# Kernel optimization log

Measured on AMD Instinct MI355X. Metric: run time of the kernel, lower is better.

The kernel has to match this reference:

```python
import jax, jax.numpy as jnp
import numpy as np

C = 256
G = 32  # GroupNorm groups
EPS = 1e-6


def setup_inputs() -> dict:
    key = jax.random.key(0)
    ks = jax.random.split(key, 10)
    b, c, d, h, w = 2, C, 16, 16, 16
    s = 1.0 / np.sqrt(c)
    return {
        "x": jax.random.normal(ks[0], (b, c, d, h, w), jnp.float32),
        "gn_gamma": jnp.ones((c,), jnp.float32),
        "gn_beta": jnp.zeros((c,), jnp.float32),
        "wq": jax.random.normal(ks[1], (c, c), jnp.float32) * s,
        "bq": jax.random.normal(ks[2], (c,), jnp.float32) * 0.01,
        "wk": jax.random.normal(ks[3], (c, c), jnp.float32) * s,
        "bk": jax.random.normal(ks[4], (c,), jnp.float32) * 0.01,
        "wv": jax.random.normal(ks[5], (c, c), jnp.float32) * s,
        "bv": jax.random.normal(ks[6], (c,), jnp.float32) * 0.01,
        "wp": jax.random.normal(ks[7], (c, c), jnp.float32) * s,
        "bp": jax.random.normal(ks[8], (c,), jnp.float32) * 0.01,
    }


def _group_norm(x, gamma, beta):
    b, c, d, h, w = x.shape
    xg = x.reshape(b, G, c // G, d, h, w)
    mu = jnp.mean(xg, axis=(2, 3, 4, 5), keepdims=True)
    var = jnp.var(xg, axis=(2, 3, 4, 5), keepdims=True)
    xn = ((xg - mu) * jax.lax.rsqrt(var + EPS)).reshape(b, c, d, h, w)
    return xn * gamma[None, :, None, None, None] + beta[None, :, None, None, None]


def reference(x, gn_gamma, gn_beta, wq, bq, wk, bk, wv, bv, wp, bp):
    b, c, d, h, w = x.shape
    n = d * h * w
    hn = _group_norm(x, gn_gamma, gn_beta).reshape(b, c, n)  # (b, c, n)
    # 1x1 conv3d == channel-mixing matmul
    q = jnp.einsum("oc,bcn->bon", wq, hn) + bq[None, :, None]
    k = jnp.einsum("oc,bcn->bon", wk, hn) + bk[None, :, None]
    v = jnp.einsum("oc,bcn->bon", wv, hn) + bv[None, :, None]
    scale = c ** (-0.5)
    attn = jax.nn.softmax(jnp.einsum("bcn,bcm->bnm", q, k) * scale, axis=2)  # (b, n, m)
    # torch: h_ = bmm(v, attn^T) -> h_[b,c,n] = sum_m v[b,c,m] * attn[b,n,m]
    hv = jnp.einsum("bcm,bnm->bcn", v, attn)
    out = jnp.einsum("oc,bcn->bon", wp, hv) + bp[None, :, None]
    w_returned = jnp.transpose(attn, (0, 2, 1))  # matches torch's returned permuted w_
    return (x + out.reshape(b, c, d, h, w), w_returned)
```

## Files before the change

### kernel.cpp

```cpp
#include <hip/hip_runtime.h>


typedef __bf16 bf16_t;
typedef __bf16 bf16x8 __attribute__((ext_vector_type(8)));
typedef float floatx4 __attribute__((ext_vector_type(4)));

__device__ __forceinline__ unsigned short f2bf(float f) {
  union { float f; unsigned int u; } v; v.f = f;
  return (unsigned short)((v.u + 0x7FFFu + ((v.u >> 16) & 1u)) >> 16);
}
__device__ __forceinline__ float bf2f(unsigned short u) {
  union { unsigned int u; float f; } v; v.u = ((unsigned int)u) << 16;
  return v.f;
}

__global__ void prep_kernel(const float* __restrict__ wq, const float* __restrict__ wk,
                            const float* __restrict__ wv, const float* __restrict__ wp,
                            const float* __restrict__ bq, const float* __restrict__ bk,
                            const float* __restrict__ bv, const float* __restrict__ bp,
                            const float* __restrict__ x, unsigned short* __restrict__ Astack,
                            unsigned short* __restrict__ wpbf, unsigned short* __restrict__ wvT,
                            float* __restrict__ bqkv2, float* __restrict__ bias2,
                            float* __restrict__ mean, float* __restrict__ rstd) {
  __shared__ float T[64 * 67];
  __shared__ float red[256];
  const int blk = blockIdx.x;
  const int tid = threadIdx.x;
  if (blk < 768) {
    int w = blk >> 8;
    const float* src = (w == 0) ? wq : (w == 1) ? wk : wp;
    unsigned short* dst = (w == 0) ? Astack : (w == 1) ? (Astack + 65536) : wpbf;
    int i = (blk & 255) * 256 + tid;
    dst[i] = f2bf(src[i]);
  } else if (blk < 784) {
    int t = blk - 768, tr = t >> 2, tc = t & 3;
#pragma unroll
    for (int rr = 0; rr < 16; ++rr) {
      int r = rr * 4 + (tid >> 6), c = tid & 63;
      T[r * 67 + c] = wv[(size_t)(tr * 64 + r) * 256 + tc * 64 + c];
    }
    __syncthreads();
#pragma unroll
    for (int rr = 0; rr < 16; ++rr) {
      int cc = rr * 4 + (tid >> 6), r = tid & 63;
      wvT[(size_t)(tc * 64 + cc) * 256 + tr * 64 + r] = f2bf(T[r * 67 + cc]);
    }
  } else if (blk < 848) {
    int bg = blk - 784;
    const float* p = x + (size_t)bg * 32768;
    float s = 0.f, ss = 0.f;
    for (int i = tid * 4; i < 32768; i += 1024) {
      float4 v = *(const float4*)&p[i];
      s += v.x + v.y + v.z + v.w;
      ss += v.x * v.x + v.y * v.y + v.z * v.z + v.w * v.w;
    }
    for (int off = 32; off > 0; off >>= 1) {
      s += __shfl_down(s, off);
      ss += __shfl_down(ss, off);
    }
    int wid = tid >> 6;
    if ((tid & 63) == 0) { red[wid] = s; red[64 + wid] = ss; }
    __syncthreads();
    if (tid == 0) {
      float S = red[0] + red[1] + red[2] + red[3];
      float SS = red[64] + red[65] + red[66] + red[67];
      float mu = S * (1.f / 32768.f);
      float var = SS * (1.f / 32768.f) - mu * mu;
      mean[bg] = mu;
      rstd[bg] = rsqrtf(var + 1e-6f);
    }
  } else if (blk == 848) {
    bqkv2[tid] = bq[tid];
    bqkv2[256 + tid] = bk[tid];
    bqkv2[512 + tid] = 0.f;
  } else {
    int bb = blk - 849;
    int o = bb * 64 + (tid >> 2), part = tid & 3;
    float s = 0.f;
#pragma unroll
    for (int j = 0; j < 16; ++j) {
      float4 w4 = *(const float4*)&wp[(size_t)o * 256 + part * 64 + j * 4];
      float4 b4 = *(const float4*)&bv[part * 64 + j * 4];
      s += w4.x * b4.x + w4.y * b4.y + w4.z * b4.z + w4.w * b4.w;
    }
    red[tid] = s;
    __syncthreads();
    if (part == 0) bias2[o] = bp[o] + red[tid] + red[tid + 1] + red[tid + 2] + red[tid + 3];
  }
}

__global__ void gn_apply_t_kernel(const float* __restrict__ x, const float* __restrict__ gamma,
                                  const float* __restrict__ beta, const float* __restrict__ mean,
                                  const float* __restrict__ rstd, unsigned short* __restrict__ hnT) {
  int n0 = blockIdx.x * 64, c0 = blockIdx.y * 64, b = blockIdx.z;
  int tid = threadIdx.x;
  __shared__ __align__(16) unsigned short T[64 * 72];
#pragma unroll
  for (int r = 0; r < 4; ++r) {
    int cl = (tid >> 4) + r * 16;
    int nl = (tid & 15) * 4;
    int c = c0 + cl;
    int bg = b * 32 + (c >> 3);
    float mu = mean[bg], rs = rstd[bg], ga = gamma[c], be = beta[c];
    float4 v = *(const float4*)&x[(size_t)b * 1048576 + (size_t)c * 4096 + n0 + nl];
    ushort4 u;
    u.x = f2bf((v.x - mu) * rs * ga + be);
    u.y = f2bf((v.y - mu) * rs * ga + be);
    u.z = f2bf((v.z - mu) * rs * ga + be);
    u.w = f2bf((v.w - mu) * rs * ga + be);
    *(ushort4*)&T[cl * 72 + nl] = u;
  }
  __syncthreads();
#pragma unroll
  for (int w = 0; w < 2; ++w) {
    int nl = (tid >> 3) + w * 32;
    int cch = (tid & 7) * 8;
    unsigned short u8[8];
#pragma unroll
    for (int i = 0; i < 8; ++i) u8[i] = T[(cch + i) * 72 + nl];
    size_t o = (size_t)b * 1048576 + (size_t)(n0 + nl) * 256 + c0 + cch;
    *(ushort4*)&hnT[o] = make_ushort4(u8[0], u8[1], u8[2], u8[3]);
    *(ushort4*)&hnT[o + 4] = make_ushort4(u8[4], u8[5], u8[6], u8[7]);
  }
}

template <int BM, int BN>
__launch_bounds__(256)
__global__ void gemm_tn(const bf16_t* __restrict__ A, const bf16_t* __restrict__ B, int ldb,
                        unsigned short* __restrict__ C, int N, int K) {
  constexpr int BK = 32, LD = BK + 8;
  constexpr int WM = BM / 2, WN = BN / 2, MI = WM / 16, NI = WN / 16;
  __shared__ __align__(16) bf16_t As[BM * LD];
  __shared__ __align__(16) bf16_t Bs[BN * LD];
  const int tid = threadIdx.x;
  const int lane = tid & 63, wid = tid >> 6;
  const int quad = lane >> 4, l16 = lane & 15;
  const int m0 = blockIdx.y * BM, n0 = blockIdx.x * BN;
  const int wm0 = (wid >> 1) * WM, wn0 = (wid & 1) * WN;

  floatx4 acc[MI][NI];
#pragma unroll
  for (int i = 0; i < MI; ++i)
#pragma unroll
    for (int j = 0; j < NI; ++j) acc[i][j] = (floatx4){0.f, 0.f, 0.f, 0.f};

  const int arow = tid >> 2, akj = (tid & 3) << 3;
  for (int kt = 0; kt < K; kt += BK) {
#pragma unroll
    for (int p = 0; p < BM / 64; ++p) {
      int r = p * 64 + arow;
      *(uint4*)&As[r * LD + akj] = *(const uint4*)&A[(size_t)(m0 + r) * K + kt + akj];
    }
#pragma unroll
    for (int p = 0; p < BN / 64; ++p) {
      int r = p * 64 + arow;
      *(uint4*)&Bs[r * LD + akj] = *(const uint4*)&B[(size_t)(n0 + r) * ldb + kt + akj];
    }
    __syncthreads();
    bf16x8 af[MI], bfr[NI];
#pragma unroll
    for (int i = 0; i < MI; ++i) af[i] = *(const bf16x8*)&As[(wm0 + i * 16 + l16) * LD + quad * 8];
#pragma unroll
    for (int j = 0; j < NI; ++j) bfr[j] = *(const bf16x8*)&Bs[(wn0 + j * 16 + l16) * LD + quad * 8];
#pragma unroll
    for (int i = 0; i < MI; ++i)
#pragma unroll
      for (int j = 0; j < NI; ++j)
        acc[i][j] = __builtin_amdgcn_mfma_f32_16x16x32_bf16(af[i], bfr[j], acc[i][j], 0, 0, 0);
    __syncthreads();
  }

#pragma unroll
  for (int i = 0; i < MI; ++i) {
    int gmb = m0 + wm0 + i * 16 + quad * 4;
#pragma unroll
    for (int j = 0; j < NI; ++j) {
      int gn = n0 + wn0 + j * 16 + l16;
#pragma unroll
      for (int r = 0; r < 4; ++r) C[(size_t)(gmb + r) * N + gn] = f2bf(acc[i][j][r]);
    }
  }
}

__launch_bounds__(256)
__global__ void gemm_qkvw(const bf16_t* __restrict__ Astack, const bf16_t* __restrict__ hnT,
                          const float* __restrict__ bqkv2, unsigned short* __restrict__ qkT,
                          unsigned short* __restrict__ W2) {
  constexpr int BM = 64, BN = 128, BK = 32, LD = BK + 8, MI = 2, NI = 4;
  __shared__ __align__(16) bf16_t As[BM * LD];
  __shared__ __align__(16) bf16_t Bs[BN * LD];
  const int tid = threadIdx.x;
  const int lane = tid & 63, wid = tid >> 6;
  const int quad = lane >> 4, l16 = lane & 15;
  const int b = blockIdx.z;
  const bf16_t* B = hnT + (size_t)b * 1048576;
  const int m0 = blockIdx.y * BM, n0 = blockIdx.x * BN;
  const int wm0 = (wid >> 1) * 32, wn0 = (wid & 1) * 64;

  floatx4 acc[MI][NI];
#pragma unroll
  for (int i = 0; i < MI; ++i)
#pragma unroll
    for (int j = 0; j < NI; ++j) acc[i][j] = (floatx4){0.f, 0.f, 0.f, 0.f};

  const int arow = tid >> 2, akj = (tid & 3) << 3;
  for (int kt = 0; kt < 256; kt += BK) {
    {
      int r = arow;
      *(uint4*)&As[r * LD + akj] = *(const uint4*)&Astack[(size_t)(m0 + r) * 256 + kt + akj];
    }
#pragma unroll
    for (int p = 0; p < 2; ++p) {
      int r = p * 64 + arow;
      *(uint4*)&Bs[r * LD + akj] = *(const uint4*)&B[(size_t)(n0 + r) * 256 + kt + akj];
    }
    __syncthreads();
    bf16x8 af[MI], bfr[NI];
#pragma unroll
    for (int i = 0; i < MI; ++i) af[i] = *(const bf16x8*)&As[(wm0 + i * 16 + l16) * LD + quad * 8];
#pragma unroll
    for (int j = 0; j < NI; ++j) bfr[j] = *(const bf16x8*)&Bs[(wn0 + j * 16 + l16) * LD + quad * 8];
#pragma unroll
    for (int i = 0; i < MI; ++i)
#pragma unroll
      for (int j = 0; j < NI; ++j)
        acc[i][j] = __builtin_amdgcn_mfma_f32_16x16x32_bf16(af[i], bfr[j], acc[i][j], 0, 0, 0);
    __syncthreads();
  }

#pragma unroll
  for (int i = 0; i < MI; ++i) {
    int gmb = m0 + wm0 + i * 16 + quad * 4;
#pragma unroll
    for (int j = 0; j < NI; ++j) {
      int gn = n0 + wn0 + j * 16 + l16;
      float v[4];
#pragma unroll
      for (int r = 0; r < 4; ++r) v[r] = acc[i][j][r] + bqkv2[gmb + r];
      if (m0 < 512) {
        ushort4 u = make_ushort4(f2bf(v[0]), f2bf(v[1]), f2bf(v[2]), f2bf(v[3]));
        *(ushort4*)&qkT[(size_t)b * 2097152 + (size_t)gn * 512 + gmb] = u;
      } else {
#pragma unroll
        for (int r = 0; r < 4; ++r)
          W2[(size_t)b * 1048576 + (size_t)(gmb - 512 + r) * 4096 + gn] = f2bf(v[r]);
      }
    }
  }
}

__launch_bounds__(256)
__global__ void gemm_qk_exp(const bf16_t* __restrict__ qkT, unsigned short* __restrict__ EbfT,
                            float* __restrict__ psum) {
  constexpr int BM = 128, BN = 128, BK = 32, LD = BK + 8, MI = 4, NI = 4;
  constexpr int LDC = BM + 8;
  __shared__ __align__(16) char SMEM[BM * LDC * 2];
  bf16_t* As = (bf16_t*)SMEM;
  bf16_t* Bs = (bf16_t*)SMEM + BM * LD;
  unsigned short* Ct = (unsigned short*)SMEM;
  const int tid = threadIdx.x;
  const int lane = tid & 63, wid = tid >> 6;
  const int quad = lane >> 4, l16 = lane & 15;
  const int b = blockIdx.z;
  const bf16_t* A = qkT + (size_t)b * 2097152 + 256;
  const bf16_t* B = qkT + (size_t)b * 2097152;
  const int m0 = blockIdx.y * BM, n0 = blockIdx.x * BN;
  const int wm0 = (wid >> 1) * 64, wn0 = (wid & 1) * 64;

  floatx4 acc[MI][NI];
#pragma unroll
  for (int i = 0; i < MI; ++i)
#pragma unroll
    for (int j = 0; j < NI; ++j) acc[i][j] = (floatx4){0.f, 0.f, 0.f, 0.f};

  const int arow = tid >> 2, akj = (tid & 3) << 3;
  for (int kt = 0; kt < 256; kt += BK) {
#pragma unroll
    for (int p = 0; p < 2; ++p) {
      int r = p * 64 + arow;
      *(uint4*)&As[r * LD + akj] = *(const uint4*)&A[(size_t)(m0 + r) * 512 + kt + akj];
      *(uint4*)&Bs[r * LD + akj] = *(const uint4*)&B[(size_t)(n0 + r) * 512 + kt + akj];
    }
    __syncthreads();
    bf16x8 af[MI], bfr[NI];
#pragma unroll
    for (int i = 0; i < MI; ++i) af[i] = *(const bf16x8*)&As[(wm0 + i * 16 + l16) * LD + quad * 8];
#pragma unroll
    for (int j = 0; j < NI; ++j) bfr[j] = *(const bf16x8*)&Bs[(wn0 + j * 16 + l16) * LD + quad * 8];
#pragma unroll
    for (int i = 0; i < MI; ++i)
#pragma unroll
      for (int j = 0; j < NI; ++j)
        acc[i][j] = __builtin_amdgcn_mfma_f32_16x16x32_bf16(af[i], bfr[j], acc[i][j], 0, 0, 0);
    __syncthreads();
  }

  float csum[NI] = {0.f, 0.f, 0.f, 0.f};
#pragma unroll
  for (int i = 0; i < MI; ++i) {
    int ml = wm0 + i * 16 + quad * 4;
#pragma unroll
    for (int j = 0; j < NI; ++j) {
      int nl = wn0 + j * 16 + l16;
      float e[4];
#pragma unroll
      for (int r = 0; r < 4; ++r) e[r] = __expf(acc[i][j][r] * 0.0625f);
      csum[j] += (e[0] + e[1]) + (e[2] + e[3]);
      *(ushort4*)&Ct[nl * LDC + ml] = make_ushort4(f2bf(e[0]), f2bf(e[1]), f2bf(e[2]), f2bf(e[3]));
    }
  }
#pragma unroll
  for (int j = 0; j < NI; ++j) {
    csum[j] += __shfl_xor(csum[j], 16);
    csum[j] += __shfl_xor(csum[j], 32);
  }
  if (quad == 0) {
    int my = blockIdx.y * 2 + (wid >> 1);
#pragma unroll
    for (int j = 0; j < NI; ++j)
      psum[((size_t)b * 64 + my) * 4096 + n0 + wn0 + j * 16 + l16] = csum[j];
  }
  __syncthreads();
#pragma unroll
  for (int pass = 0; pass < 8; ++pass) {
    int row = pass * 16 + (tid >> 4);
    int mc = (tid & 15) * 8;
    uint4 v = *(uint4*)&Ct[row * LDC + mc];
    *(uint4*)&EbfT[(size_t)b * 16777216 + (size_t)(n0 + row) * 4096 + m0 + mc] = v;
  }
}

__launch_bounds__(256)
__global__ void gemm_pv_fused(const bf16_t* __restrict__ W2, const bf16_t* __restrict__ EbfT,
                              const float* __restrict__ psum, const float* __restrict__ bias2,
                              const float* __restrict__ x, float* __restrict__ out0,
                              float* __restrict__ attn) {
  constexpr int BK = 64, LDA = 72, LDB = 72;
  __shared__ __align__(16) bf16_t As[128 * LDA];
  __shared__ __align__(16) bf16_t Bs[32 * LDB];
  __shared__ float rs[32];
  __shared__ float sred[256];
  const int tid = threadIdx.x;
  const int lane = tid & 63, wid = tid >> 6;
  const int quad = lane >> 4, l16 = lane & 15;
  const int b = blockIdx.z, mb = blockIdx.y;
  const int n0 = blockIdx.x * 32;
  const size_t eb = (size_t)b * 16777216;

  {
    int nl = tid & 31, rp = tid >> 5;
    float s = 0.f;
#pragma unroll
    for (int i = 0; i < 8; ++i) s += psum[((size_t)b * 64 + rp * 8 + i) * 4096 + n0 + nl];
    sred[tid] = s;
  }
  __syncthreads();
  if (tid < 32) {
    float s = 0.f;
#pragma unroll
    for (int i = 0; i < 8; ++i) s += sred[i * 32 + tid];
    rs[tid] = 1.f / s;
  }
  __syncthreads();

  const int wm0 = (wid >> 1) * 64, wn0 = (wid & 1) * 16;
  floatx4 acc[4];
#pragma unroll
  for (int i = 0; i < 4; ++i) acc[i] = (floatx4){0.f, 0.f, 0.f, 0.f};

  for (int kt = 0; kt < 4096; kt += BK) {
#pragma unroll
    for (int p = 0; p < 4; ++p) {
      int r = p * 32 + (tid >> 3);
      int kk = (tid & 7) * 8;
      *(uint4*)&As[r * LDA + kk] =
          *(const uint4*)&W2[(size_t)b * 1048576 + (size_t)(mb * 128 + r) * 4096 + kt + kk];
    }
    {
      int r = tid >> 3;
      int kk = (tid & 7) * 8;
      *(uint4*)&Bs[r * LDB + kk] = *(const uint4*)&EbfT[eb + (size_t)(n0 + r) * 4096 + kt + kk];
    }
    __syncthreads();
    {
      int ml = mb * 32 + (tid >> 3);
      int n4 = (tid & 7) * 4;
      const unsigned short* Bu = (const unsigned short*)Bs;
      float4 o;
      o.x = bf2f(Bu[(n4 + 0) * LDB + ml]) * rs[n4 + 0];
      o.y = bf2f(Bu[(n4 + 1) * LDB + ml]) * rs[n4 + 1];
      o.z = bf2f(Bu[(n4 + 2) * LDB + ml]) * rs[n4 + 2];
      o.w = bf2f(Bu[(n4 + 3) * LDB + ml]) * rs[n4 + 3];
      *(float4*)&attn[eb + (size_t)(kt + ml) * 4096 + n0 + n4] = o;
    }
    bf16x8 af[2][4], bfr[2];
#pragma unroll
    for (int ks = 0; ks < 2; ++ks) {
      bfr[ks] = *(const bf16x8*)&Bs[(wn0 + l16) * LDB + ks * 32 + quad * 8];
#pragma unroll
      for (int i = 0; i < 4; ++i)
        af[ks][i] = *(const bf16x8*)&As[(wm0 + i * 16 + l16) * LDA + ks * 32 + quad * 8];
    }
#pragma unroll
    for (int ks = 0; ks < 2; ++ks)
#pragma unroll
      for (int i = 0; i < 4; ++i)
        acc[i] = __builtin_amdgcn_mfma_f32_16x16x32_bf16(af[ks][i], bfr[ks], acc[i], 0, 0, 0);
    __syncthreads();
  }

  const float* xb = x + (size_t)b * 1048576;
  float* ob = out0 + (size_t)b * 1048576;
  int gn = n0 + wn0 + l16;
  float cs = rs[wn0 + l16];
#pragma unroll
  for (int i = 0; i < 4; ++i) {
    int o = mb * 128 + wm0 + i * 16 + quad * 4;
#pragma unroll
    for (int r = 0; r < 4; ++r)
      ob[(size_t)(o + r) * 4096 + gn] =
          acc[i][r] * cs + bias2[o + r] + xb[(size_t)(o + r) * 4096 + gn];
  }
}

extern "C" void kernel_launch(void* const* d_in, const int* in_sizes, int n_in,
                              void* d_out, int out_size, void* d_ws, size_t ws_size,
                              hipStream_t stream) {
  const float* x = (const float*)d_in[0];
  const float* gamma = (const float*)d_in[1];
  const float* beta = (const float*)d_in[2];
  const float* wq = (const float*)d_in[3];
  const float* bq = (const float*)d_in[4];
  const float* wk = (const float*)d_in[5];
  const float* bk = (const float*)d_in[6];
  const float* wv = (const float*)d_in[7];
  const float* bv = (const float*)d_in[8];
  const float* wp = (const float*)d_in[9];
  const float* bp = (const float*)d_in[10];

  float* out0 = (float*)d_out;
  float* attn = (float*)d_out + 2097152;

  char* ws = (char*)d_ws;
  unsigned short* Astack = (unsigned short*)(ws + 0);
  unsigned short* wpbf = (unsigned short*)(ws + 393216);
  unsigned short* wvT = (unsigned short*)(ws + 524288);
  float* bqkv2 = (float*)(ws + 655360);
  float* bias2 = (float*)(ws + 658432);
  float* gmean = (float*)(ws + 659456);
  float* grstd = (float*)(ws + 659712);
  float* psum = (float*)(ws + 1048576);
  unsigned short* hnT = (unsigned short*)(ws + 4194304);
  unsigned short* qkT = (unsigned short*)(ws + 8388608);
  unsigned short* W2 = (unsigned short*)(ws + 16777216);
  unsigned short* EbfT = (unsigned short*)(ws + 20971520);

  prep_kernel<<<853, 256, 0, stream>>>(wq, wk, wv, wp, bq, bk, bv, bp, x, Astack, wpbf, wvT,
                                       bqkv2, bias2, gmean, grstd);

  gemm_tn<64, 128><<<dim3(2, 4, 1), 256, 0, stream>>>((const bf16_t*)wpbf, (const bf16_t*)wvT, 256,
                                                      Astack + 131072, 256, 256);

  gn_apply_t_kernel<<<dim3(64, 4, 2), 256, 0, stream>>>(x, gamma, beta, gmean, grstd, hnT);

  gemm_qkvw<<<dim3(32, 12, 2), 256, 0, stream>>>((const bf16_t*)Astack, (const bf16_t*)hnT, bqkv2,
                                                 qkT, W2);

  gemm_qk_exp<<<dim3(32, 32, 2), 256, 0, stream>>>((const bf16_t*)qkT, EbfT, psum);

  gemm_pv_fused<<<dim3(128, 2, 2), 256, 0, stream>>>((const bf16_t*)W2, (const bf16_t*)EbfT, psum,
                                                     bias2, x, out0, attn);
}
```

Before: 278.0 us.

## Use direct global-to-LDS loads with XOR-swizzled tiles and larger K blocks

The three GEMM kernels now stage tiles with global_load_lds (16-byte direct-to-LDS copies) instead of loading through registers, and use XOR-swizzled unpadded LDS layouts to avoid bank conflicts. The K tile grows to 64 in the QKV and QK kernels and to 128 in the PV kernel, which halves the number of barriers per tile. The attention-weight write in the PV kernel is reindexed to read the swizzled layout and to store 8 floats per thread. This removes register staging and VGPR pressure, at the cost of more LDS use and swizzle address arithmetic.

```diff
diff --git a/kernel.cpp b/kernel.cpp
--- a/kernel.cpp
+++ b/kernel.cpp
@@ -4,6 +4,13 @@
 typedef __bf16 bf16_t;
 typedef __bf16 bf16x8 __attribute__((ext_vector_type(8)));
 typedef float floatx4 __attribute__((ext_vector_type(4)));
+
+typedef __attribute__((address_space(1))) const unsigned int gas_u32;
+typedef __attribute__((address_space(3))) unsigned int las_u32;
+
+__device__ __forceinline__ void gl_lds16(const void* g, void* l) {
+  __builtin_amdgcn_global_load_lds((gas_u32*)g, (las_u32*)l, 16, 0, 0);
+}
 
 __device__ __forceinline__ unsigned short f2bf(float f) {
   union { float f; unsigned int u; } v; v.f = f;
@@ -101,13 +108,13 @@
     int nl = (tid & 15) * 4;
     int c = c0 + cl;
     int bg = b * 32 + (c >> 3);
-    float mu = mean[bg], rs = rstd[bg], ga = gamma[c], be = beta[c];
+    float mu = mean[bg], rsd = rstd[bg], ga = gamma[c], be = beta[c];
     float4 v = *(const float4*)&x[(size_t)b * 1048576 + (size_t)c * 4096 + n0 + nl];
     ushort4 u;
-    u.x = f2bf((v.x - mu) * rs * ga + be);
-    u.y = f2bf((v.y - mu) * rs * ga + be);
-    u.z = f2bf((v.z - mu) * rs * ga + be);
-    u.w = f2bf((v.w - mu) * rs * ga + be);
+    u.x = f2bf((v.x - mu) * rsd * ga + be);
+    u.y = f2bf((v.y - mu) * rsd * ga + be);
+    u.z = f2bf((v.z - mu) * rsd * ga + be);
+    u.w = f2bf((v.w - mu) * rsd * ga + be);
     *(ushort4*)&T[cl * 72 + nl] = u;
   }
   __syncthreads();
@@ -186,9 +193,9 @@
 __global__ void gemm_qkvw(const bf16_t* __restrict__ Astack, const bf16_t* __restrict__ hnT,
                           const float* __restrict__ bqkv2, unsigned short* __restrict__ qkT,
                           unsigned short* __restrict__ W2) {
-  constexpr int BM = 64, BN = 128, BK = 32, LD = BK + 8, MI = 2, NI = 4;
-  __shared__ __align__(16) bf16_t As[BM * LD];
-  __shared__ __align__(16) bf16_t Bs[BN * LD];
+  constexpr int BM = 64, BN = 128, BK = 64, MI = 2, NI = 4;
+  __shared__ __align__(16) bf16_t As[BM * BK];
+  __shared__ __align__(16) bf16_t Bs[BN * BK];
   const int tid = threadIdx.x;
   const int lane = tid & 63, wid = tid >> 6;
   const int quad = lane >> 4, l16 = lane & 15;
@@ -196,6 +203,8 @@
   const bf16_t* B = hnT + (size_t)b * 1048576;
   const int m0 = blockIdx.y * BM, n0 = blockIdx.x * BN;
   const int wm0 = (wid >> 1) * 32, wn0 = (wid & 1) * 64;
+  const int srow = lane >> 3;
+  const int scol = ((lane & 7) ^ srow) << 3;
 
   floatx4 acc[MI][NI];
 #pragma unroll
@@ -203,28 +212,37 @@
 #pragma unroll
     for (int j = 0; j < NI; ++j) acc[i][j] = (floatx4){0.f, 0.f, 0.f, 0.f};
 
-  const int arow = tid >> 2, akj = (tid & 3) << 3;
   for (int kt = 0; kt < 256; kt += BK) {
-    {
-      int r = arow;
-      *(uint4*)&As[r * LD + akj] = *(const uint4*)&Astack[(size_t)(m0 + r) * 256 + kt + akj];
-    }
 #pragma unroll
     for (int p = 0; p < 2; ++p) {
-      int r = p * 64 + arow;
-      *(uint4*)&Bs[r * LD + akj] = *(const uint4*)&B[(size_t)(n0 + r) * 256 + kt + akj];
-    }
-    __syncthreads();
-    bf16x8 af[MI], bfr[NI];
-#pragma unroll
-    for (int i = 0; i < MI; ++i) af[i] = *(const bf16x8*)&As[(wm0 + i * 16 + l16) * LD + quad * 8];
-#pragma unroll
-    for (int j = 0; j < NI; ++j) bfr[j] = *(const bf16x8*)&Bs[(wn0 + j * 16 + l16) * LD + quad * 8];
-#pragma unroll
-    for (int i = 0; i < MI; ++i)
-#pragma unroll
-      for (int j = 0; j < NI; ++j)
-        acc[i][j] = __builtin_amdgcn_mfma_f32_16x16x32_bf16(af[i], bfr[j], acc[i][j], 0, 0, 0);
+      int rb = wid * 16 + p * 8;
+      gl_lds16(&Astack[(size_t)(m0 + rb + srow) * 256 + kt + scol], &As[rb * BK]);
+    }
+#pragma unroll
+    for (int p = 0; p < 4; ++p) {
+      int rb = wid * 32 + p * 8;
+      gl_lds16(&B[(size_t)(n0 + rb + srow) * 256 + kt + scol], &Bs[rb * BK]);
+    }
+    __syncthreads();
+#pragma unroll
+    for (int ks = 0; ks < 2; ++ks) {
+      bf16x8 af[MI], bfr[NI];
+#pragma unroll
+      for (int i = 0; i < MI; ++i) {
+        int r = wm0 + i * 16 + l16;
+        af[i] = *(const bf16x8*)&As[r * BK + ((((ks << 2) + quad) ^ (r & 7)) << 3)];
+      }
+#pragma unroll
+      for (int j = 0; j < NI; ++j) {
+        int r = wn0 + j * 16 + l16;
+        bfr[j] = *(const bf16x8*)&Bs[r * BK + ((((ks << 2) + quad) ^ (r & 7)) << 3)];
+      }
+#pragma unroll
+      for (int i = 0; i < MI; ++i)
+#pragma unroll
+        for (int j = 0; j < NI; ++j)
+          acc[i][j] = __builtin_amdgcn_mfma_f32_16x16x32_bf16(af[i], bfr[j], acc[i][j], 0, 0, 0);
+    }
     __syncthreads();
   }
 
@@ -252,11 +270,11 @@
 __launch_bounds__(256)
 __global__ void gemm_qk_exp(const bf16_t* __restrict__ qkT, unsigned short* __restrict__ EbfT,
                             float* __restrict__ psum) {
-  constexpr int BM = 128, BN = 128, BK = 32, LD = BK + 8, MI = 4, NI = 4;
+  constexpr int BM = 128, BN = 128, BK = 64, MI = 4, NI = 4;
   constexpr int LDC = BM + 8;
   __shared__ __align__(16) char SMEM[BM * LDC * 2];
   bf16_t* As = (bf16_t*)SMEM;
-  bf16_t* Bs = (bf16_t*)SMEM + BM * LD;
+  bf16_t* Bs = (bf16_t*)SMEM + BM * BK;
   unsigned short* Ct = (unsigned short*)SMEM;
   const int tid = threadIdx.x;
   const int lane = tid & 63, wid = tid >> 6;
@@ -266,6 +284,8 @@
   const bf16_t* B = qkT + (size_t)b * 2097152;
   const int m0 = blockIdx.y * BM, n0 = blockIdx.x * BN;
   const int wm0 = (wid >> 1) * 64, wn0 = (wid & 1) * 64;
+  const int srow = lane >> 3;
+  const int scol = ((lane & 7) ^ srow) << 3;
 
   floatx4 acc[MI][NI];
 #pragma unroll
@@ -273,25 +293,33 @@
 #pragma unroll
     for (int j = 0; j < NI; ++j) acc[i][j] = (floatx4){0.f, 0.f, 0.f, 0.f};
 
-  const int arow = tid >> 2, akj = (tid & 3) << 3;
   for (int kt = 0; kt < 256; kt += BK) {
 #pragma unroll
-    for (int p = 0; p < 2; ++p) {
-      int r = p * 64 + arow;
-      *(uint4*)&As[r * LD + akj] = *(const uint4*)&A[(size_t)(m0 + r) * 512 + kt + akj];
-      *(uint4*)&Bs[r * LD + akj] = *(const uint4*)&B[(size_t)(n0 + r) * 512 + kt + akj];
-    }
-    __syncthreads();
-    bf16x8 af[MI], bfr[NI];
-#pragma unroll
-    for (int i = 0; i < MI; ++i) af[i] = *(const bf16x8*)&As[(wm0 + i * 16 + l16) * LD + quad * 8];
-#pragma unroll
-    for (int j = 0; j < NI; ++j) bfr[j] = *(const bf16x8*)&Bs[(wn0 + j * 16 + l16) * LD + quad * 8];
-#pragma unroll
-    for (int i = 0; i < MI; ++i)
-#pragma unroll
-      for (int j = 0; j < NI; ++j)
-        acc[i][j] = __builtin_amdgcn_mfma_f32_16x16x32_bf16(af[i], bfr[j], acc[i][j], 0, 0, 0);
+    for (int p = 0; p < 4; ++p) {
+      int rb = wid * 32 + p * 8;
+      gl_lds16(&A[(size_t)(m0 + rb + srow) * 512 + kt + scol], &As[rb * BK]);
+      gl_lds16(&B[(size_t)(n0 + rb + srow) * 512 + kt + scol], &Bs[rb * BK]);
+    }
+    __syncthreads();
+#pragma unroll
+    for (int ks = 0; ks < 2; ++ks) {
+      bf16x8 af[MI], bfr[NI];
+#pragma unroll
+      for (int i = 0; i < MI; ++i) {
+        int r = wm0 + i * 16 + l16;
+        af[i] = *(const bf16x8*)&As[r * BK + ((((ks << 2) + quad) ^ (r & 7)) << 3)];
+      }
+#pragma unroll
+      for (int j = 0; j < NI; ++j) {
+        int r = wn0 + j * 16 + l16;
+        bfr[j] = *(const bf16x8*)&Bs[r * BK + ((((ks << 2) + quad) ^ (r & 7)) << 3)];
+      }
+#pragma unroll
+      for (int i = 0; i < MI; ++i)
+#pragma unroll
+        for (int j = 0; j < NI; ++j)
+          acc[i][j] = __builtin_amdgcn_mfma_f32_16x16x32_bf16(af[i], bfr[j], acc[i][j], 0, 0, 0);
+    }
     __syncthreads();
   }
 
@@ -335,9 +363,9 @@
                               const float* __restrict__ psum, const float* __restrict__ bias2,
                               const float* __restrict__ x, float* __restrict__ out0,
                               float* __restrict__ attn) {
-  constexpr int BK = 64, LDA = 72, LDB = 72;
-  __shared__ __align__(16) bf16_t As[128 * LDA];
-  __shared__ __align__(16) bf16_t Bs[32 * LDB];
+  constexpr int BK = 128;
+  __shared__ __align__(16) bf16_t As[128 * BK];
+  __shared__ __align__(16) bf16_t Bs[32 * BK];
   __shared__ float rs[32];
   __shared__ float sred[256];
   const int tid = threadIdx.x;
@@ -364,48 +392,53 @@
   __syncthreads();
 
   const int wm0 = (wid >> 1) * 64, wn0 = (wid & 1) * 16;
+  const int r4 = lane >> 4, s16 = lane & 15;
+  const bf16_t* Wb = W2 + (size_t)b * 1048576 + (size_t)(mb * 128) * 4096;
+  const bf16_t* Eb = EbfT + eb;
+  const int pml = mb * 64 + (tid >> 2);
+  const int pn4 = (tid & 3) * 8;
+
   floatx4 acc[4];
 #pragma unroll
   for (int i = 0; i < 4; ++i) acc[i] = (floatx4){0.f, 0.f, 0.f, 0.f};
 
   for (int kt = 0; kt < 4096; kt += BK) {
 #pragma unroll
-    for (int p = 0; p < 4; ++p) {
-      int r = p * 32 + (tid >> 3);
-      int kk = (tid & 7) * 8;
-      *(uint4*)&As[r * LDA + kk] =
-          *(const uint4*)&W2[(size_t)b * 1048576 + (size_t)(mb * 128 + r) * 4096 + kt + kk];
-    }
+    for (int p = 0; p < 8; ++p) {
+      int rb = wid * 32 + p * 4;
+      int key = ((p & 1) << 2) | r4;
+      gl_lds16(&Wb[(size_t)(rb + r4) * 4096 + kt + ((s16 ^ key) << 3)], &As[rb * BK]);
+    }
+#pragma unroll
+    for (int p = 0; p < 2; ++p) {
+      int rb = wid * 8 + p * 4;
+      int key = ((p & 1) << 2) | r4;
+      gl_lds16(&Eb[(size_t)(n0 + rb + r4) * 4096 + kt + ((s16 ^ key) << 3)], &Bs[rb * BK]);
+    }
+    __syncthreads();
     {
-      int r = tid >> 3;
-      int kk = (tid & 7) * 8;
-      *(uint4*)&Bs[r * LDB + kk] = *(const uint4*)&EbfT[eb + (size_t)(n0 + r) * 4096 + kt + kk];
-    }
-    __syncthreads();
-    {
-      int ml = mb * 32 + (tid >> 3);
-      int n4 = (tid & 7) * 4;
       const unsigned short* Bu = (const unsigned short*)Bs;
-      float4 o;
-      o.x = bf2f(Bu[(n4 + 0) * LDB + ml]) * rs[n4 + 0];
-      o.y = bf2f(Bu[(n4 + 1) * LDB + ml]) * rs[n4 + 1];
-      o.z = bf2f(Bu[(n4 + 2) * LDB + ml]) * rs[n4 + 2];
-      o.w = bf2f(Bu[(n4 + 3) * LDB + ml]) * rs[n4 + 3];
-      *(float4*)&attn[eb + (size_t)(kt + ml) * 4096 + n0 + n4] = o;
-    }
-    bf16x8 af[2][4], bfr[2];
-#pragma unroll
-    for (int ks = 0; ks < 2; ++ks) {
-      bfr[ks] = *(const bf16x8*)&Bs[(wn0 + l16) * LDB + ks * 32 + quad * 8];
-#pragma unroll
-      for (int i = 0; i < 4; ++i)
-        af[ks][i] = *(const bf16x8*)&As[(wm0 + i * 16 + l16) * LDA + ks * 32 + quad * 8];
-    }
-#pragma unroll
-    for (int ks = 0; ks < 2; ++ks)
-#pragma unroll
-      for (int i = 0; i < 4; ++i)
-        acc[i] = __builtin_amdgcn_mfma_f32_16x16x32_bf16(af[ks][i], bfr[ks], acc[i], 0, 0, 0);
+      float o[8];
+#pragma unroll
+      for (int j = 0; j < 8; ++j) {
+        int n = pn4 + j;
+        o[j] = bf2f(Bu[n * BK + ((((pml >> 3) ^ (n & 7)) << 3) | (pml & 7))]) * rs[n];
+      }
+      size_t ro = eb + (size_t)(kt + pml) * 4096 + n0 + pn4;
+      *(float4*)&attn[ro] = make_float4(o[0], o[1], o[2], o[3]);
+      *(float4*)&attn[ro + 4] = make_float4(o[4], o[5], o[6], o[7]);
+    }
+#pragma unroll
+    for (int ks = 0; ks < 4; ++ks) {
+      int rn = wn0 + l16;
+      bf16x8 bfr = *(const bf16x8*)&Bs[rn * BK + ((((ks << 2) + quad) ^ (rn & 7)) << 3)];
+#pragma unroll
+      for (int i = 0; i < 4; ++i) {
+        int rm = wm0 + i * 16 + l16;
+        bf16x8 af = *(const bf16x8*)&As[rm * BK + ((((ks << 2) + quad) ^ (rm & 7)) << 3)];
+        acc[i] = __builtin_amdgcn_mfma_f32_16x16x32_bf16(af, bfr, acc[i], 0, 0, 0);
+      }
+    }
     __syncthreads();
   }
 
```

After: 263.0 us. 1.06x faster.
